# Kernel tuning notes

Measured on AMD Instinct MI355X. Metric: run time of the kernel, lower is better.

## Reference

```python
import jax, jax.numpy as jnp
import numpy as np

B, C, D, E, ES, TOPK = 8, 4096, 1024, 16, 256, 4096

def setup_inputs() -> dict:
    key = jax.random.key(0)
    k1, k2, k3, k4 = jax.random.split(key, 4)
    x = jax.random.normal(k1, (B, C, D), dtype=jnp.float32)
    gate = jax.random.normal(k2, (C, E), dtype=jnp.float32) / np.sqrt(D)
    lin1_weight = jax.random.normal(k3, (D, E, ES), dtype=jnp.float32) / np.sqrt(D)
    lin2_weight = jax.random.normal(k4, (E, ES, D), dtype=jnp.float32) / np.sqrt(ES)
    return {"x": x, "gate": gate, "lin1_weight": lin1_weight, "lin2_weight": lin2_weight, "topk": TOPK}

def reference(x, gate, lin1_weight, lin2_weight, topk):
    b, c, d = x.shape
    e = gate.shape[1]
    n_tokens = b * c
    # faithful to original einsum: sum x over dmodel, elementwise-mult by gate[c, e]
    gate_out = jnp.einsum('bcd,ce->bce', x, gate)            # [b, c, e]
    gate_out = jnp.transpose(gate_out, (2, 0, 1)).reshape(e, n_tokens)
    gate_out = jax.nn.softmax(gate_out, axis=1)              # softmax over tokens per expert
    topk_values, topk_indices = jax.lax.top_k(gate_out, topk)  # [e, k]
    xf = x.reshape(n_tokens, d)
    flat_idx = topk_indices.reshape(-1)
    gathered = xf[flat_idx].reshape(e, topk, d)              # dispatch
    h = jax.nn.relu(jnp.einsum('ekd,des->eks', gathered, lin1_weight))
    out = jnp.einsum('eks,esd->ekd', h, lin2_weight)
    out = out * topk_values[..., None]                       # weight by gate probs
    z = jnp.zeros_like(xf).at[flat_idx].add(out.reshape(-1, d))  # scatter-add combine
    return z.reshape(b, c, d)
```

## Files before the change

kernel.cpp:

```cpp
#include <hip/hip_runtime.h>
#include <hip/hip_bf16.h>

#define BB 8
#define CC 4096
#define DD 1024
#define EE 16
#define ESS 256
#define KSEL 4096
#define NTOK (BB*CC)

typedef short bf16x8 __attribute__((ext_vector_type(8)));
typedef float f32x4 __attribute__((ext_vector_type(4)));

struct PickRes { unsigned tau; unsigned n_gt; unsigned n_tie; float sm; };

__device__ __forceinline__ short f2bf(float f) {
  unsigned u = __float_as_uint(f);
  u += 0x7FFFu + ((u >> 16) & 1u);
  return (short)(u >> 16);
}
__device__ __forceinline__ float bf2f(short s) {
  return __uint_as_float(((unsigned)(unsigned short)s) << 16);
}
__device__ __forceinline__ unsigned f2key(float f) {
  unsigned u = __float_as_uint(f);
  return (u & 0x80000000u) ? ~u : (u | 0x80000000u);
}

#define ASG __attribute__((address_space(1)))
#define ASL __attribute__((address_space(3)))
__device__ __forceinline__ void gl_lds16(void* l, const void* g) {
  __builtin_amdgcn_global_load_lds((ASG const unsigned*)g, (ASL unsigned*)l, 16, 0, 0);
}

__global__ void k_logits(const float* __restrict__ x, const float* __restrict__ gate,
                         float* __restrict__ logits, short* __restrict__ xb) {
  int wid = threadIdx.x >> 6, lane = threadIdx.x & 63;
  int t = blockIdx.x * 4 + wid;
  const float4* xr = reinterpret_cast<const float4*>(x + (size_t)t * DD);
  short4* xw = reinterpret_cast<short4*>(xb + (size_t)t * DD);
  float s = 0.f;
#pragma unroll
  for (int i = 0; i < 4; ++i) {
    float4 v = xr[lane + 64 * i];
    s += v.x + v.y + v.z + v.w;
    short4 p;
    p.x = f2bf(v.x); p.y = f2bf(v.y); p.z = f2bf(v.z); p.w = f2bf(v.w);
    xw[lane + 64 * i] = p;
  }
#pragma unroll
  for (int off = 32; off; off >>= 1) s += __shfl_xor(s, off);
  if (lane < EE) {
    int c = t & (CC - 1);
    logits[(size_t)lane * NTOK + t] = s * gate[c * EE + lane];
  }
}

__global__ __launch_bounds__(1024) void k_hist(const float* __restrict__ logits,
                                               unsigned* __restrict__ ghist,
                                               float* __restrict__ separt) {
  int e = blockIdx.x & 15, seg = blockIdx.x >> 4;
  const float* L = logits + (size_t)e * NTOK + seg * 4096;
  unsigned* Hh = ghist + (size_t)e * 65536;
  int tid = threadIdx.x;
  float sl = 0.f;
#pragma unroll
  for (int i = 0; i < 4; ++i) {
    float lv = L[tid + 1024 * i];
    atomicAdd(&Hh[f2key(lv) >> 16], 1u);
    sl += expf(lv);
  }
  __shared__ float red[1024];
  red[tid] = sl; __syncthreads();
  for (int s2 = 512; s2; s2 >>= 1) {
    if (tid < s2) red[tid] += red[tid + s2];
    __syncthreads();
  }
  if (tid == 0) separt[e * 8 + seg] = red[0];
}

__global__ __launch_bounds__(1024) void k_pick(const unsigned* __restrict__ ghist,
                                               const float* __restrict__ logits,
                                               const float* __restrict__ separt,
                                               PickRes* __restrict__ pres) {
  int e = blockIdx.x;
  const unsigned* Hh = ghist + (size_t)e * 65536;
  const float* L = logits + (size_t)e * NTOK;
  int tid = threadIdx.x;
  __shared__ unsigned u0[1024], u1[1024];
  __shared__ unsigned hist256[256];
  __shared__ unsigned sh_b16, sh_ngt, sh_kth;
  __shared__ unsigned sh_p24, sh_ngt2, sh_kth2;

  unsigned cs = 0;
  for (int j = 0; j < 64; ++j) cs += Hh[tid * 64 + j];
  u0[tid] = cs; __syncthreads();
  unsigned* src = u0; unsigned* dst = u1;
  for (int d2 = 1; d2 < 1024; d2 <<= 1) {
    unsigned v = src[tid] + ((tid + d2 < 1024) ? src[tid + d2] : 0u);
    dst[tid] = v; __syncthreads();
    unsigned* tmp = src; src = dst; dst = tmp;
  }
  unsigned kth0 = KSEL;
  unsigned above = (tid < 1023) ? src[tid + 1] : 0u;
  if (above < kth0 && kth0 <= src[tid]) {
    unsigned cum = above;
    for (int j = 63; j >= 0; --j) {
      unsigned h = Hh[tid * 64 + j];
      if (cum + h >= kth0) { sh_b16 = (unsigned)(tid * 64 + j); sh_ngt = cum; sh_kth = kth0 - cum; break; }
      cum += h;
    }
  }
  __syncthreads();
  unsigned p16 = sh_b16, ngt1 = sh_ngt, kth1 = sh_kth;

  if (tid < 256) hist256[tid] = 0;
  __syncthreads();
  for (int t = tid; t < NTOK; t += 1024) {
    unsigned key = f2key(L[t]);
    if ((key >> 16) == p16) atomicAdd(&hist256[(key >> 8) & 255], 1u);
  }
  __syncthreads();
  if (tid == 0) {
    unsigned cum = 0; int d = 255;
    for (; d >= 0; --d) { unsigned h = hist256[d]; if (cum + h >= kth1) break; cum += h; }
    sh_p24 = (p16 << 8) | (unsigned)d;
    sh_ngt2 = ngt1 + cum;
    sh_kth2 = kth1 - cum;
  }
  __syncthreads();
  unsigned p24 = sh_p24, ngt2 = sh_ngt2, kth2 = sh_kth2;

  if (tid < 256) hist256[tid] = 0;
  __syncthreads();
  for (int t = tid; t < NTOK; t += 1024) {
    unsigned key = f2key(L[t]);
    if ((key >> 8) == p24) atomicAdd(&hist256[key & 255], 1u);
  }
  __syncthreads();
  if (tid == 0) {
    unsigned cum = 0; int d = 255;
    for (; d >= 0; --d) { unsigned h = hist256[d]; if (cum + h >= kth2) break; cum += h; }
    unsigned tau = (p24 << 8) | (unsigned)d;
    unsigned n_gt = ngt2 + cum;
    float sm = 0.f;
    for (int j = 0; j < 8; ++j) sm += separt[e * 8 + j];
    PickRes pr; pr.tau = tau; pr.n_gt = n_gt; pr.n_tie = KSEL - n_gt; pr.sm = sm;
    pres[e] = pr;
  }
}

__global__ __launch_bounds__(1024) void k_count(const float* __restrict__ logits,
                                                const PickRes* __restrict__ pres,
                                                unsigned* __restrict__ cnts) {
  int e = blockIdx.x & 15, seg = blockIdx.x >> 4;
  PickRes pr = pres[e];
  const float* L = logits + (size_t)e * NTOK + seg * 4096;
  int tid = threadIdx.x;
  unsigned pk = 0;
#pragma unroll
  for (int i = 0; i < 4; ++i) {
    unsigned key = f2key(L[tid + 1024 * i]);
    pk += (key > pr.tau) ? 0x10000u : ((key == pr.tau) ? 1u : 0u);
  }
  __shared__ unsigned red[1024];
  red[tid] = pk; __syncthreads();
  for (int s2 = 512; s2; s2 >>= 1) {
    if (tid < s2) red[tid] += red[tid + s2];
    __syncthreads();
  }
  if (tid == 0) cnts[e * 8 + seg] = red[0];
}

__global__ void k_scan(const unsigned* __restrict__ cnts, unsigned* __restrict__ bases) {
  int e = threadIdx.x;
  if (e < EE) {
    unsigned gb = 0, qb = 0;
    for (int s = 0; s < 8; ++s) {
      unsigned c = cnts[e * 8 + s];
      bases[e * 8 + s] = (gb << 16) | qb;
      gb += c >> 16; qb += c & 0xFFFFu;
    }
  }
}

__global__ __launch_bounds__(1024) void k_compact(const float* __restrict__ logits,
                                                  const PickRes* __restrict__ pres,
                                                  const unsigned* __restrict__ bases,
                                                  int* __restrict__ sel_idx,
                                                  float* __restrict__ sel_val,
                                                  int* __restrict__ inv) {
  int e = blockIdx.x & 15, seg = blockIdx.x >> 4;
  PickRes pr = pres[e];
  const float* L = logits + (size_t)e * NTOK;
  unsigned b = bases[e * 8 + seg];
  __shared__ unsigned wtg[16], wtq[16];
  __shared__ unsigned base_g, base_q;
  int tid = threadIdx.x, wid = tid >> 6, lane = tid & 63;
  if (tid == 0) { base_g = b >> 16; base_q = b & 0xFFFFu; }
  __syncthreads();
#pragma unroll 1
  for (int i = 0; i < 4; ++i) {
    int t = seg * 4096 + tid + 1024 * i;
    float lv = L[t];
    unsigned key = f2key(lv);
    bool g = key > pr.tau, q = key == pr.tau;
    unsigned long long bg = __ballot(g), bq = __ballot(q);
    unsigned long long lm = (1ull << lane) - 1ull;
    unsigned pg = __popcll(bg & lm), pq = __popcll(bq & lm);
    if (lane == 63) { wtg[wid] = pg + (g ? 1u : 0u); wtq[wid] = pq + (q ? 1u : 0u); }
    __syncthreads();
    unsigned og = base_g, oq = base_q;
    for (int w2 = 0; w2 < wid; ++w2) { og += wtg[w2]; oq += wtq[w2]; }
    unsigned slot = 0xFFFFFFFFu;
    if (g) slot = og + pg;
    else if (q) {
      unsigned r = oq + pq;
      if (r < pr.n_tie) slot = pr.n_gt + r;
    }
    if (slot != 0xFFFFFFFFu) {
      sel_idx[(size_t)e * KSEL + slot] = t;
      sel_val[(size_t)e * KSEL + slot] = expf(lv) / pr.sm;
      inv[(size_t)t * EE + e] = e * KSEL + (int)slot;
    }
    __syncthreads();
    if (tid == 0) {
      unsigned sg = 0, sq = 0;
#pragma unroll
      for (int w2 = 0; w2 < 16; ++w2) { sg += wtg[w2]; sq += wtq[w2]; }
      base_g += sg; base_q += sq;
    }
    __syncthreads();
  }
}

__global__ void k_transpose(const float* __restrict__ src, short* __restrict__ dst,
                            int R, int C) {
  __shared__ float tile[64][65];
  int c0 = blockIdx.x * 64, r0 = blockIdx.y * 64, b = blockIdx.z;
  const float* S = src + (size_t)b * R * C;
  short* Dp = dst + (size_t)b * R * C;
  int tx = threadIdx.x & 63, ty = threadIdx.x >> 6;
#pragma unroll
  for (int i = 0; i < 16; ++i) {
    int r = ty + 4 * i;
    tile[r][tx] = S[(size_t)(r0 + r) * C + c0 + tx];
  }
  __syncthreads();
#pragma unroll
  for (int i = 0; i < 16; ++i) {
    int cR = ty + 4 * i;
    Dp[(size_t)(c0 + cR) * R + r0 + tx] = f2bf(tile[tx][cR]);
  }
}

__global__ __launch_bounds__(512, 1) void k_gemm1(
    const short* __restrict__ xb, const short* __restrict__ W1T,
    const int* __restrict__ sel_idx, const float* __restrict__ sel_val,
    short* __restrict__ H) {
  int bid = blockIdx.x;
  int m0 = ((bid >> 3) & 31) * 128;
  int e = (bid & 7) + ((bid >> 8) << 3);
  __shared__ bf16x8 As8[2 * 128 * 8];
  __shared__ bf16x8 Bs8[2 * 256 * 8];
  int tid = threadIdx.x, lane = tid & 63, wid = tid >> 6;
  int wr = wid >> 2, wc = wid & 3;
  const int* idxE = sel_idx + (size_t)e * KSEL;
  f32x4 acc[4][4] = {};

  int rowA = tid >> 3, sA = tid & 7;
  int xk = rowA & 7;
  const short* aSrc0 = xb + (size_t)idxE[m0 + rowA] * DD + (sA ^ xk) * 8;
  const short* aSrc1 = xb + (size_t)idxE[m0 + rowA + 64] * DD + (sA ^ xk) * 8;
  const short* wBase = W1T + (size_t)e * ESS * DD + (size_t)rowA * DD + (sA ^ xk) * 8;

  auto stage = [&](int b, int kt) {
    int kofs = kt * 64;
    gl_lds16(&As8[b * 1024 + tid], aSrc0 + kofs);
    gl_lds16(&As8[b * 1024 + 512 + tid], aSrc1 + kofs);
#pragma unroll
    for (int j = 0; j < 4; ++j)
      gl_lds16(&Bs8[b * 2048 + j * 512 + tid], wBase + (size_t)(64 * j) * DD + kofs);
  };

  stage(0, 0);
  __syncthreads();
  for (int kt = 0; kt < DD / 64; ++kt) {
    int cur = kt & 1;
    if (kt < DD / 64 - 1) stage(cur ^ 1, kt + 1);
    bf16x8 af[4][2];
#pragma unroll
    for (int mg = 0; mg < 4; ++mg) {
      int row = wr * 64 + mg * 16 + (lane & 15);
#pragma unroll
      for (int h = 0; h < 2; ++h) {
        int seg = h * 4 + (lane >> 4);
        af[mg][h] = As8[cur * 1024 + row * 8 + (seg ^ (row & 7))];
      }
    }
#pragma unroll
    for (int ng = 0; ng < 4; ++ng) {
      int rowb = wc * 64 + ng * 16 + (lane & 15);
      bf16x8 b0 = Bs8[cur * 2048 + rowb * 8 + (((lane >> 4) + 0) ^ (rowb & 7))];
      bf16x8 b1 = Bs8[cur * 2048 + rowb * 8 + (((lane >> 4) + 4) ^ (rowb & 7))];
#pragma unroll
      for (int mg = 0; mg < 4; ++mg) {
        acc[mg][ng] = __builtin_amdgcn_mfma_f32_16x16x32_bf16(af[mg][0], b0, acc[mg][ng], 0, 0, 0);
        acc[mg][ng] = __builtin_amdgcn_mfma_f32_16x16x32_bf16(af[mg][1], b1, acc[mg][ng], 0, 0, 0);
      }
    }
    __syncthreads();
  }
#pragma unroll
  for (int mg = 0; mg < 4; ++mg) {
#pragma unroll
    for (int r = 0; r < 4; ++r) {
      int ml = wr * 64 + mg * 16 + (lane >> 4) * 4 + r;
      float v = sel_val[(size_t)e * KSEL + m0 + ml];
#pragma unroll
      for (int ng = 0; ng < 4; ++ng) {
        float o = fmaxf(acc[mg][ng][r], 0.f) * v;
        H[((size_t)(e * KSEL + m0 + ml)) * ESS + wc * 64 + ng * 16 + (lane & 15)] = f2bf(o);
      }
    }
  }
}

template <int COMBINE>
__global__ __launch_bounds__(512, 1) void k_gemm2(
    const short* __restrict__ H, const short* __restrict__ W2T,
    const int* __restrict__ sel_idx, float* __restrict__ z, short* __restrict__ out) {
  int bid = blockIdx.x;
  int p = (bid & 7) + ((bid >> 8) << 3);
  int m0 = ((bid >> 3) & 31) * 128;
  int n0 = (p & 3) * 256;
  int e = p >> 2;
  __shared__ bf16x8 As8[2 * 128 * 8];
  __shared__ bf16x8 Bs8[2 * 256 * 8];
  int tid = threadIdx.x, lane = tid & 63, wid = tid >> 6;
  int wr = wid >> 2, wc = wid & 3;
  f32x4 acc[4][4] = {};

  int rowA = tid >> 3, sA = tid & 7;
  int xk = rowA & 7;
  const short* hBase = H + (size_t)(e * KSEL + m0 + rowA) * ESS + (sA ^ xk) * 8;
  const short* w2Base = W2T + (size_t)(e * DD + n0 + rowA) * ESS + (sA ^ xk) * 8;

  auto stage = [&](int b, int kt) {
    int kofs = kt * 64;
    gl_lds16(&As8[b * 1024 + tid], hBase + kofs);
    gl_lds16(&As8[b * 1024 + 512 + tid], hBase + (size_t)64 * ESS + kofs);
#pragma unroll
    for (int j = 0; j < 4; ++j)
      gl_lds16(&Bs8[b * 2048 + j * 512 + tid], w2Base + (size_t)(64 * j) * ESS + kofs);
  };

  stage(0, 0);
  __syncthreads();
  for (int kt = 0; kt < ESS / 64; ++kt) {
    int cur = kt & 1;
    if (kt < ESS / 64 - 1) stage(cur ^ 1, kt + 1);
    bf16x8 af[4][2];
#pragma unroll
    for (int mg = 0; mg < 4; ++mg) {
      int row = wr * 64 + mg * 16 + (lane & 15);
#pragma unroll
      for (int h = 0; h < 2; ++h) {
        int seg = h * 4 + (lane >> 4);
        af[mg][h] = As8[cur * 1024 + row * 8 + (seg ^ (row & 7))];
      }
    }
#pragma unroll
    for (int ng = 0; ng < 4; ++ng) {
      int rowb = wc * 64 + ng * 16 + (lane & 15);
      bf16x8 b0 = Bs8[cur * 2048 + rowb * 8 + (((lane >> 4) + 0) ^ (rowb & 7))];
      bf16x8 b1 = Bs8[cur * 2048 + rowb * 8 + (((lane >> 4) + 4) ^ (rowb & 7))];
#pragma unroll
      for (int mg = 0; mg < 4; ++mg) {
        acc[mg][ng] = __builtin_amdgcn_mfma_f32_16x16x32_bf16(af[mg][0], b0, acc[mg][ng], 0, 0, 0);
        acc[mg][ng] = __builtin_amdgcn_mfma_f32_16x16x32_bf16(af[mg][1], b1, acc[mg][ng], 0, 0, 0);
      }
    }
    __syncthreads();
  }
#pragma unroll
  for (int mg = 0; mg < 4; ++mg) {
#pragma unroll
    for (int r = 0; r < 4; ++r) {
      int ml = wr * 64 + mg * 16 + (lane >> 4) * 4 + r;
      if (COMBINE) {
        short* orow = out + ((size_t)(e * KSEL + m0 + ml)) * DD + n0 + wc * 64 + (lane & 15);
#pragma unroll
        for (int ng = 0; ng < 4; ++ng) orow[ng * 16] = f2bf(acc[mg][ng][r]);
      } else {
        int token = sel_idx[(size_t)e * KSEL + m0 + ml];
        float* zr = z + (size_t)token * DD + n0 + wc * 64 + (lane & 15);
#pragma unroll
        for (int ng = 0; ng < 4; ++ng) atomicAdd(zr + ng * 16, acc[mg][ng][r]);
      }
    }
  }
}

__global__ void k_combine(const short* __restrict__ out, const int* __restrict__ inv,
                          float* __restrict__ z) {
  int wid = threadIdx.x >> 6, lane = threadIdx.x & 63;
  int t = blockIdx.x * 4 + wid;
  int g[16];
  const int4* iv4 = reinterpret_cast<const int4*>(inv + (size_t)t * EE);
#pragma unroll
  for (int q = 0; q < 4; ++q) {
    int4 v = iv4[q];
    g[4 * q] = v.x; g[4 * q + 1] = v.y; g[4 * q + 2] = v.z; g[4 * q + 3] = v.w;
  }
  float acc[16] = {};
#pragma unroll
  for (int e = 0; e < EE; ++e) {
    if (g[e] < 0) continue;
    const uint4* rp = reinterpret_cast<const uint4*>(out + (size_t)g[e] * DD + lane * 16);
    uint4 v0 = rp[0], v1 = rp[1];
    const short* s0 = reinterpret_cast<const short*>(&v0);
    const short* s1 = reinterpret_cast<const short*>(&v1);
#pragma unroll
    for (int i = 0; i < 8; ++i) acc[i] += bf2f(s0[i]);
#pragma unroll
    for (int i = 0; i < 8; ++i) acc[8 + i] += bf2f(s1[i]);
  }
  float4* zw = reinterpret_cast<float4*>(z + (size_t)t * DD + lane * 16);
#pragma unroll
  for (int i = 0; i < 4; ++i) {
    float4 o; o.x = acc[4 * i]; o.y = acc[4 * i + 1]; o.z = acc[4 * i + 2]; o.w = acc[4 * i + 3];
    zw[i] = o;
  }
}

extern "C" void kernel_launch(void* const* d_in, const int* in_sizes, int n_in,
                              void* d_out, int out_size, void* d_ws, size_t ws_size,
                              hipStream_t stream) {
  (void)in_sizes; (void)n_in;
  const float* x = (const float*)d_in[0];
  const float* gate = (const float*)d_in[1];
  const float* lin1 = (const float*)d_in[2];
  const float* lin2 = (const float*)d_in[3];
  float* z = (float*)d_out;

  char* ws = (char*)d_ws;
  size_t off = 0;
  auto alloc = [&](size_t bytes) -> void* {
    off = (off + 255) & ~(size_t)255;
    void* p = ws + off;
    off += bytes;
    return p;
  };
  float* logits = (float*)alloc((size_t)EE * NTOK * 4);
  int* sidx = (int*)alloc((size_t)EE * KSEL * 4);
  float* sval = (float*)alloc((size_t)EE * KSEL * 4);
  int* inv = (int*)alloc((size_t)NTOK * EE * 4);
  short* W1T = (short*)alloc((size_t)EE * ESS * DD * 2);
  short* W2T = (short*)alloc((size_t)EE * DD * ESS * 2);
  short* H = (short*)alloc((size_t)EE * KSEL * ESS * 2);
  short* xb = (short*)alloc((size_t)NTOK * DD * 2);
  size_t out_bytes = (size_t)EE * KSEL * DD * 2;
  bool combine = (off + 256 + out_bytes) <= ws_size;
  short* outbuf = combine ? (short*)alloc(out_bytes) : nullptr;

  unsigned* ghist = (unsigned*)H;
  float* separt = (float*)((char*)H + (size_t)EE * 65536 * 4);
  PickRes* pres = (PickRes*)((char*)separt + 1024);
  unsigned* cnts = (unsigned*)((char*)pres + 1024);
  unsigned* bases = (unsigned*)((char*)cnts + 1024);

  k_transpose<<<dim3(64, 16, 1), 256, 0, stream>>>(lin1, W1T, DD, EE * ESS);
  k_transpose<<<dim3(16, 4, 16), 256, 0, stream>>>(lin2, W2T, ESS, DD);
  k_logits<<<NTOK / 4, 256, 0, stream>>>(x, gate, logits, xb);
  hipMemsetAsync(inv, 0xFF, (size_t)NTOK * EE * 4, stream);
  hipMemsetAsync(ghist, 0, (size_t)EE * 65536 * 4, stream);
  k_hist<<<128, 1024, 0, stream>>>(logits, ghist, separt);
  k_pick<<<EE, 1024, 0, stream>>>(ghist, logits, separt, pres);
  k_count<<<128, 1024, 0, stream>>>(logits, pres, cnts);
  k_scan<<<1, 64, 0, stream>>>(cnts, bases);
  k_compact<<<128, 1024, 0, stream>>>(logits, pres, bases, sidx, sval, inv);
  k_gemm1<<<512, 512, 0, stream>>>(xb, W1T, sidx, sval, H);
  if (combine) {
    k_gemm2<1><<<2048, 512, 0, stream>>>(H, W2T, sidx, z, outbuf);
    k_combine<<<NTOK / 4, 256, 0, stream>>>(outbuf, inv, z);
  } else {
    hipMemsetAsync(d_out, 0, (size_t)out_size * sizeof(float), stream);
    k_gemm2<0><<<2048, 512, 0, stream>>>(H, W2T, sidx, z, nullptr);
  }
}
```

Measured before the change: 359.9 us.

## Single-buffer GEMM LDS for higher occupancy, nontemporal stores, fuse inv init

Both GEMM kernels drop double-buffered LDS staging for a single buffer with a sync after each load, and launch bounds rise to 4 blocks per CU so more workgroups can hide latency. Streaming outputs (xb, H, expert outputs, z) and the combine-kernel reads switch to nontemporal loads and stores. The inv -1 initialization moves into k_logits, removing a memset. The trade is that load/compute overlap inside each block is lost, and capping registers for 4 blocks may cause spills.

```diff
diff --git a/kernel.cpp b/kernel.cpp
--- a/kernel.cpp
+++ b/kernel.cpp
@@ -11,6 +11,8 @@
 
 typedef short bf16x8 __attribute__((ext_vector_type(8)));
 typedef float f32x4 __attribute__((ext_vector_type(4)));
+typedef short s16x4 __attribute__((ext_vector_type(4)));
+typedef unsigned u32x4 __attribute__((ext_vector_type(4)));
 
 struct PickRes { unsigned tau; unsigned n_gt; unsigned n_tie; float sm; };
 
@@ -34,25 +36,27 @@
 }
 
 __global__ void k_logits(const float* __restrict__ x, const float* __restrict__ gate,
-                         float* __restrict__ logits, short* __restrict__ xb) {
+                         float* __restrict__ logits, short* __restrict__ xb,
+                         int* __restrict__ inv) {
   int wid = threadIdx.x >> 6, lane = threadIdx.x & 63;
   int t = blockIdx.x * 4 + wid;
   const float4* xr = reinterpret_cast<const float4*>(x + (size_t)t * DD);
-  short4* xw = reinterpret_cast<short4*>(xb + (size_t)t * DD);
+  s16x4* xw = reinterpret_cast<s16x4*>(xb + (size_t)t * DD);
   float s = 0.f;
 #pragma unroll
   for (int i = 0; i < 4; ++i) {
     float4 v = xr[lane + 64 * i];
     s += v.x + v.y + v.z + v.w;
-    short4 p;
-    p.x = f2bf(v.x); p.y = f2bf(v.y); p.z = f2bf(v.z); p.w = f2bf(v.w);
-    xw[lane + 64 * i] = p;
+    s16x4 p;
+    p[0] = f2bf(v.x); p[1] = f2bf(v.y); p[2] = f2bf(v.z); p[3] = f2bf(v.w);
+    __builtin_nontemporal_store(p, &xw[lane + 64 * i]);
   }
 #pragma unroll
   for (int off = 32; off; off >>= 1) s += __shfl_xor(s, off);
   if (lane < EE) {
     int c = t & (CC - 1);
     logits[(size_t)lane * NTOK + t] = s * gate[c * EE + lane];
+    inv[(size_t)t * EE + lane] = -1;
   }
 }
 
@@ -254,15 +258,15 @@
   }
 }
 
-__global__ __launch_bounds__(512, 1) void k_gemm1(
+__global__ __launch_bounds__(512, 4) void k_gemm1(
     const short* __restrict__ xb, const short* __restrict__ W1T,
     const int* __restrict__ sel_idx, const float* __restrict__ sel_val,
     short* __restrict__ H) {
   int bid = blockIdx.x;
   int m0 = ((bid >> 3) & 31) * 128;
   int e = (bid & 7) + ((bid >> 8) << 3);
-  __shared__ bf16x8 As8[2 * 128 * 8];
-  __shared__ bf16x8 Bs8[2 * 256 * 8];
+  __shared__ bf16x8 As8[128 * 8];
+  __shared__ bf16x8 Bs8[256 * 8];
   int tid = threadIdx.x, lane = tid & 63, wid = tid >> 6;
   int wr = wid >> 2, wc = wid & 3;
   const int* idxE = sel_idx + (size_t)e * KSEL;
@@ -274,20 +278,14 @@
   const short* aSrc1 = xb + (size_t)idxE[m0 + rowA + 64] * DD + (sA ^ xk) * 8;
   const short* wBase = W1T + (size_t)e * ESS * DD + (size_t)rowA * DD + (sA ^ xk) * 8;
 
-  auto stage = [&](int b, int kt) {
+  for (int kt = 0; kt < DD / 64; ++kt) {
     int kofs = kt * 64;
-    gl_lds16(&As8[b * 1024 + tid], aSrc0 + kofs);
-    gl_lds16(&As8[b * 1024 + 512 + tid], aSrc1 + kofs);
+    gl_lds16(&As8[tid], aSrc0 + kofs);
+    gl_lds16(&As8[512 + tid], aSrc1 + kofs);
 #pragma unroll
     for (int j = 0; j < 4; ++j)
-      gl_lds16(&Bs8[b * 2048 + j * 512 + tid], wBase + (size_t)(64 * j) * DD + kofs);
-  };
-
-  stage(0, 0);
-  __syncthreads();
-  for (int kt = 0; kt < DD / 64; ++kt) {
-    int cur = kt & 1;
-    if (kt < DD / 64 - 1) stage(cur ^ 1, kt + 1);
+      gl_lds16(&Bs8[j * 512 + tid], wBase + (size_t)(64 * j) * DD + kofs);
+    __syncthreads();
     bf16x8 af[4][2];
 #pragma unroll
     for (int mg = 0; mg < 4; ++mg) {
@@ -295,14 +293,14 @@
 #pragma unroll
       for (int h = 0; h < 2; ++h) {
         int seg = h * 4 + (lane >> 4);
-        af[mg][h] = As8[cur * 1024 + row * 8 + (seg ^ (row & 7))];
+        af[mg][h] = As8[row * 8 + (seg ^ (row & 7))];
       }
     }
 #pragma unroll
     for (int ng = 0; ng < 4; ++ng) {
       int rowb = wc * 64 + ng * 16 + (lane & 15);
-      bf16x8 b0 = Bs8[cur * 2048 + rowb * 8 + (((lane >> 4) + 0) ^ (rowb & 7))];
-      bf16x8 b1 = Bs8[cur * 2048 + rowb * 8 + (((lane >> 4) + 4) ^ (rowb & 7))];
+      bf16x8 b0 = Bs8[rowb * 8 + (((lane >> 4) + 0) ^ (rowb & 7))];
+      bf16x8 b1 = Bs8[rowb * 8 + (((lane >> 4) + 4) ^ (rowb & 7))];
 #pragma unroll
       for (int mg = 0; mg < 4; ++mg) {
         acc[mg][ng] = __builtin_amdgcn_mfma_f32_16x16x32_bf16(af[mg][0], b0, acc[mg][ng], 0, 0, 0);
@@ -317,17 +315,18 @@
     for (int r = 0; r < 4; ++r) {
       int ml = wr * 64 + mg * 16 + (lane >> 4) * 4 + r;
       float v = sel_val[(size_t)e * KSEL + m0 + ml];
+      short* hrow = H + ((size_t)(e * KSEL + m0 + ml)) * ESS + wc * 64 + (lane & 15);
 #pragma unroll
       for (int ng = 0; ng < 4; ++ng) {
         float o = fmaxf(acc[mg][ng][r], 0.f) * v;
-        H[((size_t)(e * KSEL + m0 + ml)) * ESS + wc * 64 + ng * 16 + (lane & 15)] = f2bf(o);
+        __builtin_nontemporal_store(f2bf(o), hrow + ng * 16);
       }
     }
   }
 }
 
 template <int COMBINE>
-__global__ __launch_bounds__(512, 1) void k_gemm2(
+__global__ __launch_bounds__(512, 4) void k_gemm2(
     const short* __restrict__ H, const short* __restrict__ W2T,
     const int* __restrict__ sel_idx, float* __restrict__ z, short* __restrict__ out) {
   int bid = blockIdx.x;
@@ -335,8 +334,8 @@
   int m0 = ((bid >> 3) & 31) * 128;
   int n0 = (p & 3) * 256;
   int e = p >> 2;
-  __shared__ bf16x8 As8[2 * 128 * 8];
-  __shared__ bf16x8 Bs8[2 * 256 * 8];
+  __shared__ bf16x8 As8[128 * 8];
+  __shared__ bf16x8 Bs8[256 * 8];
   int tid = threadIdx.x, lane = tid & 63, wid = tid >> 6;
   int wr = wid >> 2, wc = wid & 3;
   f32x4 acc[4][4] = {};
@@ -346,20 +345,14 @@
   const short* hBase = H + (size_t)(e * KSEL + m0 + rowA) * ESS + (sA ^ xk) * 8;
   const short* w2Base = W2T + (size_t)(e * DD + n0 + rowA) * ESS + (sA ^ xk) * 8;
 
-  auto stage = [&](int b, int kt) {
+  for (int kt = 0; kt < ESS / 64; ++kt) {
     int kofs = kt * 64;
-    gl_lds16(&As8[b * 1024 + tid], hBase + kofs);
-    gl_lds16(&As8[b * 1024 + 512 + tid], hBase + (size_t)64 * ESS + kofs);
+    gl_lds16(&As8[tid], hBase + kofs);
+    gl_lds16(&As8[512 + tid], hBase + (size_t)64 * ESS + kofs);
 #pragma unroll
     for (int j = 0; j < 4; ++j)
-      gl_lds16(&Bs8[b * 2048 + j * 512 + tid], w2Base + (size_t)(64 * j) * ESS + kofs);
-  };
-
-  stage(0, 0);
-  __syncthreads();
-  for (int kt = 0; kt < ESS / 64; ++kt) {
-    int cur = kt & 1;
-    if (kt < ESS / 64 - 1) stage(cur ^ 1, kt + 1);
+      gl_lds16(&Bs8[j * 512 + tid], w2Base + (size_t)(64 * j) * ESS + kofs);
+    __syncthreads();
     bf16x8 af[4][2];
 #pragma unroll
     for (int mg = 0; mg < 4; ++mg) {
@@ -367,14 +360,14 @@
 #pragma unroll
       for (int h = 0; h < 2; ++h) {
         int seg = h * 4 + (lane >> 4);
-        af[mg][h] = As8[cur * 1024 + row * 8 + (seg ^ (row & 7))];
+        af[mg][h] = As8[row * 8 + (seg ^ (row & 7))];
       }
     }
 #pragma unroll
     for (int ng = 0; ng < 4; ++ng) {
       int rowb = wc * 64 + ng * 16 + (lane & 15);
-      bf16x8 b0 = Bs8[cur * 2048 + rowb * 8 + (((lane >> 4) + 0) ^ (rowb & 7))];
-      bf16x8 b1 = Bs8[cur * 2048 + rowb * 8 + (((lane >> 4) + 4) ^ (rowb & 7))];
+      bf16x8 b0 = Bs8[rowb * 8 + (((lane >> 4) + 0) ^ (rowb & 7))];
+      bf16x8 b1 = Bs8[rowb * 8 + (((lane >> 4) + 4) ^ (rowb & 7))];
 #pragma unroll
       for (int mg = 0; mg < 4; ++mg) {
         acc[mg][ng] = __builtin_amdgcn_mfma_f32_16x16x32_bf16(af[mg][0], b0, acc[mg][ng], 0, 0, 0);
@@ -391,7 +384,8 @@
       if (COMBINE) {
         short* orow = out + ((size_t)(e * KSEL + m0 + ml)) * DD + n0 + wc * 64 + (lane & 15);
 #pragma unroll
-        for (int ng = 0; ng < 4; ++ng) orow[ng * 16] = f2bf(acc[mg][ng][r]);
+        for (int ng = 0; ng < 4; ++ng)
+          __builtin_nontemporal_store(f2bf(acc[mg][ng][r]), orow + ng * 16);
       } else {
         int token = sel_idx[(size_t)e * KSEL + m0 + ml];
         float* zr = z + (size_t)token * DD + n0 + wc * 64 + (lane & 15);
@@ -417,8 +411,9 @@
 #pragma unroll
   for (int e = 0; e < EE; ++e) {
     if (g[e] < 0) continue;
-    const uint4* rp = reinterpret_cast<const uint4*>(out + (size_t)g[e] * DD + lane * 16);
-    uint4 v0 = rp[0], v1 = rp[1];
+    const u32x4* rp = reinterpret_cast<const u32x4*>(out + (size_t)g[e] * DD + lane * 16);
+    u32x4 v0 = __builtin_nontemporal_load(rp);
+    u32x4 v1 = __builtin_nontemporal_load(rp + 1);
     const short* s0 = reinterpret_cast<const short*>(&v0);
     const short* s1 = reinterpret_cast<const short*>(&v1);
 #pragma unroll
@@ -426,11 +421,12 @@
 #pragma unroll
     for (int i = 0; i < 8; ++i) acc[8 + i] += bf2f(s1[i]);
   }
-  float4* zw = reinterpret_cast<float4*>(z + (size_t)t * DD + lane * 16);
+  f32x4* zw = reinterpret_cast<f32x4*>(z + (size_t)t * DD + lane * 16);
 #pragma unroll
   for (int i = 0; i < 4; ++i) {
-    float4 o; o.x = acc[4 * i]; o.y = acc[4 * i + 1]; o.z = acc[4 * i + 2]; o.w = acc[4 * i + 3];
-    zw[i] = o;
+    f32x4 o;
+    o[0] = acc[4 * i]; o[1] = acc[4 * i + 1]; o[2] = acc[4 * i + 2]; o[3] = acc[4 * i + 3];
+    __builtin_nontemporal_store(o, &zw[i]);
   }
 }
 
@@ -472,8 +468,7 @@
 
   k_transpose<<<dim3(64, 16, 1), 256, 0, stream>>>(lin1, W1T, DD, EE * ESS);
   k_transpose<<<dim3(16, 4, 16), 256, 0, stream>>>(lin2, W2T, ESS, DD);
-  k_logits<<<NTOK / 4, 256, 0, stream>>>(x, gate, logits, xb);
-  hipMemsetAsync(inv, 0xFF, (size_t)NTOK * EE * 4, stream);
+  k_logits<<<NTOK / 4, 256, 0, stream>>>(x, gate, logits, xb, inv);
   hipMemsetAsync(ghist, 0, (size_t)EE * 65536 * 4, stream);
   k_hist<<<128, 1024, 0, stream>>>(logits, ghist, separt);
   k_pick<<<EE, 1024, 0, stream>>>(ghist, logits, separt, pres);
```

New measurement: 345.0 us. 1.04x faster.
